# Kernel optimization log

Hardware: AMD Instinct MI355X
Metric: run time of the kernel (lower is better)

Reference implementation:

```python
import jax, jax.numpy as jnp
import numpy as np

B, SIZE, OUT = 32, 2048, 2048
EPS = 1e-5

def setup_inputs() -> dict:
    key = jax.random.key(0)
    ks = jax.random.split(key, 6)
    s = SIZE ** -0.5
    return {
        "x":    jax.random.normal(ks[0], (B, SIZE), jnp.float32),
        "Wq":   jax.random.normal(ks[1], (SIZE, SIZE), jnp.float32) * s,
        "Wk":   jax.random.normal(ks[2], (SIZE, SIZE), jnp.float32) * s,
        "Wv":   jax.random.normal(ks[3], (SIZE, SIZE), jnp.float32) * s,
        "p2":   jnp.zeros((5,), jnp.float32),              # OptimActivation params (activation2)
        "Wfc2": jax.random.normal(ks[4], (OUT, SIZE), jnp.float32) * s,
        "bfc2": jnp.zeros((OUT,), jnp.float32),
        "g2":   jnp.ones((OUT,), jnp.float32),             # LayerNorm2 weight
        "b2":   jnp.zeros((OUT,), jnp.float32),            # LayerNorm2 bias
    }

def _optim_activation(x, p):
    ps = jax.nn.softmax(p)
    # swish + sine + linear branches (sigmoid/tanh branches are computed but not summed in the original)
    return jax.nn.sigmoid(x) * x * ps[0] + jnp.sin(x) * ps[1] + x * ps[2]

def _layernorm(x, g, b):
    mu = jnp.mean(x, axis=-1, keepdims=True)
    var = jnp.mean(jnp.square(x - mu), axis=-1, keepdims=True)
    return (x - mu) * jax.lax.rsqrt(var + EPS) * g + b

def reference(x, Wq, Wk, Wv, p2, Wfc2, bfc2, g2, b2):
    q = x @ Wq.T                                   # [B, S]
    k = x @ Wk.T
    v = x @ Wv.T
    bsz, s = x.shape
    att = q[:, :, None] * k[:, None, :]            # outer product  [B, S, S]
    att = jax.nn.softmax(att.reshape(bsz, s * s), axis=-1).reshape(bsz, s, s)
    valued = jnp.einsum('bij,bj->bi', att, v)      # [B, S]
    # NOTE: original's activation/fc_linear/norm result is overwritten (dead code)
    fc = _optim_activation(valued, p2)
    fc = fc @ Wfc2.T + bfc2                        # [B, OUT]
    return _layernorm(fc, g2, b2)
```

## Files before the change

kernel.cpp:

```cpp
#include <hip/hip_runtime.h>
#include <hip/hip_bf16.h>


#define S 2048
#define BATCH 32

typedef __attribute__((ext_vector_type(8))) short short8;
typedef __attribute__((ext_vector_type(4))) float f32x4;

__device__ __forceinline__ void cvt8t(const float* __restrict__ p, short8& hi, short8& lo) {
  const float4* p4 = (const float4*)p;
  float4 a = p4[0], b = p4[1];
  float v[8] = {a.x, a.y, a.z, a.w, b.x, b.y, b.z, b.w};
#pragma unroll
  for (int t = 0; t < 8; ++t) {
    union { float f; unsigned u; } x; x.f = v[t];
    unsigned hb = x.u & 0xFFFF0000u;
    hi[t] = (short)(x.u >> 16);
    union { unsigned u; float f; } h; h.u = hb;
    union { float f; unsigned u; } l; l.f = v[t] - h.f;
    lo[t] = (short)(l.u >> 16);
  }
}

__global__ __launch_bounds__(512) void k_qkv(
    const float* __restrict__ x,
    const float* __restrict__ Wq,
    const float* __restrict__ Wk,
    const float* __restrict__ Wv,
    float* __restrict__ qkv) {
  int mi   = blockIdx.x >> 7;
  int nblk = blockIdx.x & 127;
  const float* W = (mi == 0) ? Wq : (mi == 1) ? Wk : Wv;
  float* out = qkv + mi * (BATCH * S);

  int tid  = threadIdx.x;
  int wave = tid >> 6;
  int lane = tid & 63;
  int lr   = lane & 15;
  int quad = lane >> 4;

  f32x4 acc0 = {0.f, 0.f, 0.f, 0.f};
  f32x4 acc1 = {0.f, 0.f, 0.f, 0.f};
  const float* wrow = W + (size_t)(nblk * 16 + lr) * S;
  const float* xr0  = x + (size_t)lr * S;
  const float* xr1  = x + (size_t)(lr + 16) * S;
  int kbase = wave * 256 + quad * 8;

#pragma unroll 2
  for (int ks = 0; ks < 8; ++ks) {
    int k0 = kbase + ks * 32;
    short8 bhi, blo, a0h, a0l, a1h, a1l;
    cvt8t(wrow + k0, bhi, blo);
    cvt8t(xr0 + k0, a0h, a0l);
    cvt8t(xr1 + k0, a1h, a1l);
    acc0 = __builtin_amdgcn_mfma_f32_16x16x32_bf16(a0h, bhi, acc0, 0, 0, 0);
    acc0 = __builtin_amdgcn_mfma_f32_16x16x32_bf16(a0l, bhi, acc0, 0, 0, 0);
    acc0 = __builtin_amdgcn_mfma_f32_16x16x32_bf16(a0h, blo, acc0, 0, 0, 0);
    acc1 = __builtin_amdgcn_mfma_f32_16x16x32_bf16(a1h, bhi, acc1, 0, 0, 0);
    acc1 = __builtin_amdgcn_mfma_f32_16x16x32_bf16(a1l, bhi, acc1, 0, 0, 0);
    acc1 = __builtin_amdgcn_mfma_f32_16x16x32_bf16(a1h, blo, acc1, 0, 0, 0);
  }

  __shared__ float red[8][64][8];
#pragma unroll
  for (int r = 0; r < 4; ++r) {
    red[wave][lane][r]     = acc0[r];
    red[wave][lane][4 + r] = acc1[r];
  }
  __syncthreads();
  if (tid < 64) {
    int lq = tid >> 4, lc = tid & 15;
    int n = nblk * 16 + lc;
#pragma unroll
    for (int r = 0; r < 8; ++r) {
      float s = 0.f;
#pragma unroll
      for (int w = 0; w < 8; ++w) s += red[w][tid][r];
      int m = (r < 4) ? (lq * 4 + r) : (16 + lq * 4 + (r - 4));
      out[m * S + n] = s;
    }
  }
}

__global__ __launch_bounds__(256) void k_attn(
    const float* __restrict__ qkv, float* __restrict__ Tout, float* __restrict__ Z) {
  int b    = blockIdx.x >> 5;
  int iblk = blockIdx.x & 31;
  const float* q = qkv + b * S;
  const float* k = qkv + BATCH * S + b * S;
  const float* v = qkv + 2 * BATCH * S + b * S;

  __shared__ __align__(16) float2 kv[S];
  __shared__ float redmx[4][4];
  __shared__ float redST[256][2];
  __shared__ float Msh;

  int tid = threadIdx.x;
  float qmx = -1e30f, qmn = 1e30f, kmx = -1e30f, kmn = 1e30f;
  for (int idx = tid; idx < S; idx += 256) {
    float kk = k[idx], vv = v[idx], qq = q[idx];
    kv[idx] = make_float2(kk, vv);
    qmx = fmaxf(qmx, qq); qmn = fminf(qmn, qq);
    kmx = fmaxf(kmx, kk); kmn = fminf(kmn, kk);
  }
  for (int off = 32; off; off >>= 1) {
    qmx = fmaxf(qmx, __shfl_xor(qmx, off));
    qmn = fminf(qmn, __shfl_xor(qmn, off));
    kmx = fmaxf(kmx, __shfl_xor(kmx, off));
    kmn = fminf(kmn, __shfl_xor(kmn, off));
  }
  int wave = tid >> 6, lane = tid & 63;
  if (lane == 0) {
    redmx[wave][0] = qmx; redmx[wave][1] = qmn;
    redmx[wave][2] = kmx; redmx[wave][3] = kmn;
  }
  __syncthreads();
  if (tid == 0) {
    float a = redmx[0][0], bn = redmx[0][1], c = redmx[0][2], d = redmx[0][3];
    for (int w = 1; w < 4; ++w) {
      a = fmaxf(a, redmx[w][0]); bn = fminf(bn, redmx[w][1]);
      c = fmaxf(c, redmx[w][2]); d = fminf(d, redmx[w][3]);
    }
    Msh = fmaxf(fmaxf(a * c, a * d), fmaxf(bn * c, bn * d));
  }
  __syncthreads();
  float M = Msh;

  const float LOG2E = 1.4426950408889634f;
  int i = iblk * 64 + lane;
  float aa = q[i] * LOG2E;
  float cc = -M * LOG2E;
  float Sacc = 0.f, Tacc = 0.f;
  int j0 = wave * 512;
#pragma unroll 8
  for (int j = j0; j < j0 + 512; j += 2) {
    float4 p = *(const float4*)&kv[j];
    float e0 = __builtin_amdgcn_exp2f(fmaf(aa, p.x, cc));
    float e1 = __builtin_amdgcn_exp2f(fmaf(aa, p.z, cc));
    Sacc += e0 + e1;
    Tacc = fmaf(e0, p.y, fmaf(e1, p.w, Tacc));
  }
  redST[tid][0] = Sacc;
  redST[tid][1] = Tacc;
  __syncthreads();
  if (tid < 64) {
    float Sf = redST[tid][0] + redST[tid + 64][0] + redST[tid + 128][0] + redST[tid + 192][0];
    float Tf = redST[tid][1] + redST[tid + 64][1] + redST[tid + 128][1] + redST[tid + 192][1];
    Tout[b * S + iblk * 64 + tid] = Tf;
    for (int off = 32; off; off >>= 1) Sf += __shfl_xor(Sf, off);
    if (tid == 0) atomicAdd(&Z[b], Sf);
  }
}

__global__ __launch_bounds__(256) void k_act(
    const float* __restrict__ Tin, const float* __restrict__ Z,
    const float* __restrict__ p2, float* __restrict__ fc) {
  int gid = blockIdx.x * 256 + threadIdx.x;
  int b = gid >> 11;
  const float LOG2E = 1.4426950408889634f;
  float p[5];
  float mx = -1e30f;
#pragma unroll
  for (int t = 0; t < 5; ++t) { p[t] = p2[t]; mx = fmaxf(mx, p[t]); }
  float se = 0.f;
#pragma unroll
  for (int t = 0; t < 5; ++t) { p[t] = __builtin_amdgcn_exp2f((p[t] - mx) * LOG2E); se += p[t]; }
  float inv = 1.f / se;
  float val = Tin[gid] / Z[b];
  float sig = __builtin_amdgcn_rcpf(1.f + __builtin_amdgcn_exp2f(-val * LOG2E));
  float sn  = __builtin_amdgcn_sinf(val * 0.15915494309189535f);
  fc[gid] = sig * val * (p[0] * inv) + sn * (p[1] * inv) + val * (p[2] * inv);
}

__global__ __launch_bounds__(512) void k_fc(
    const float* __restrict__ fc,
    const float* __restrict__ W,
    const float* __restrict__ bias,
    float* __restrict__ y) {
  int nblk = blockIdx.x;
  int tid  = threadIdx.x;
  int wave = tid >> 6;
  int lane = tid & 63;
  int lr   = lane & 15;
  int quad = lane >> 4;

  f32x4 acc0 = {0.f, 0.f, 0.f, 0.f};
  f32x4 acc1 = {0.f, 0.f, 0.f, 0.f};
  const float* wrow = W + (size_t)(nblk * 16 + lr) * S;
  const float* xr0  = fc + (size_t)lr * S;
  const float* xr1  = fc + (size_t)(lr + 16) * S;
  int kbase = wave * 256 + quad * 8;

#pragma unroll 2
  for (int ks = 0; ks < 8; ++ks) {
    int k0 = kbase + ks * 32;
    short8 bhi, blo, a0h, a0l, a1h, a1l;
    cvt8t(wrow + k0, bhi, blo);
    cvt8t(xr0 + k0, a0h, a0l);
    cvt8t(xr1 + k0, a1h, a1l);
    acc0 = __builtin_amdgcn_mfma_f32_16x16x32_bf16(a0h, bhi, acc0, 0, 0, 0);
    acc0 = __builtin_amdgcn_mfma_f32_16x16x32_bf16(a0l, bhi, acc0, 0, 0, 0);
    acc0 = __builtin_amdgcn_mfma_f32_16x16x32_bf16(a0h, blo, acc0, 0, 0, 0);
    acc1 = __builtin_amdgcn_mfma_f32_16x16x32_bf16(a1h, bhi, acc1, 0, 0, 0);
    acc1 = __builtin_amdgcn_mfma_f32_16x16x32_bf16(a1l, bhi, acc1, 0, 0, 0);
    acc1 = __builtin_amdgcn_mfma_f32_16x16x32_bf16(a1h, blo, acc1, 0, 0, 0);
  }

  __shared__ float red[8][64][8];
#pragma unroll
  for (int r = 0; r < 4; ++r) {
    red[wave][lane][r]     = acc0[r];
    red[wave][lane][4 + r] = acc1[r];
  }
  __syncthreads();
  if (tid < 64) {
    int lq = tid >> 4, lc = tid & 15;
    int n = nblk * 16 + lc;
    float bsum = bias[n];
#pragma unroll
    for (int r = 0; r < 8; ++r) {
      float s = 0.f;
#pragma unroll
      for (int w = 0; w < 8; ++w) s += red[w][tid][r];
      int m = (r < 4) ? (lq * 4 + r) : (16 + lq * 4 + (r - 4));
      y[m * S + n] = s + bsum;
    }
  }
}

__global__ __launch_bounds__(256) void k_ln(
    const float* __restrict__ y, const float* __restrict__ g,
    const float* __restrict__ bb, float* __restrict__ out) {
  int b = blockIdx.x;
  const float* row = y + b * S;
  float s = 0.f, s2 = 0.f;
  for (int i = threadIdx.x; i < S; i += 256) {
    float t = row[i];
    s += t; s2 += t * t;
  }
  for (int off = 32; off; off >>= 1) {
    s  += __shfl_xor(s, off);
    s2 += __shfl_xor(s2, off);
  }
  __shared__ float rs[4], rs2[4];
  __shared__ float mu_s, r_s;
  int wave = threadIdx.x >> 6, lane = threadIdx.x & 63;
  if (lane == 0) { rs[wave] = s; rs2[wave] = s2; }
  __syncthreads();
  if (threadIdx.x == 0) {
    float S1 = rs[0] + rs[1] + rs[2] + rs[3];
    float S2 = rs2[0] + rs2[1] + rs2[2] + rs2[3];
    float mu = S1 / (float)S;
    float var = S2 / (float)S - mu * mu;
    mu_s = mu;
    r_s = rsqrtf(var + 1e-5f);
  }
  __syncthreads();
  float mu = mu_s, r = r_s;
  for (int i = threadIdx.x; i < S; i += 256) {
    out[b * S + i] = (row[i] - mu) * r * g[i] + bb[i];
  }
}

extern "C" void kernel_launch(void* const* d_in, const int* in_sizes, int n_in,
                              void* d_out, int out_size, void* d_ws, size_t ws_size,
                              hipStream_t stream) {
  (void)in_sizes; (void)n_in; (void)out_size; (void)ws_size;
  const float* x    = (const float*)d_in[0];
  const float* Wq   = (const float*)d_in[1];
  const float* Wk   = (const float*)d_in[2];
  const float* Wv   = (const float*)d_in[3];
  const float* p2   = (const float*)d_in[4];
  const float* Wfc2 = (const float*)d_in[5];
  const float* bfc2 = (const float*)d_in[6];
  const float* g2   = (const float*)d_in[7];
  const float* b2   = (const float*)d_in[8];
  float* out = (float*)d_out;

  float* qkv = (float*)d_ws;
  float* T   = qkv + 3 * BATCH * S;
  float* Z   = T + BATCH * S;
  float* fc  = Z + 32;
  float* y   = fc + BATCH * S;

  hipMemsetAsync(Z, 0, 32 * sizeof(float), stream);
  k_qkv<<<384, 512, 0, stream>>>(x, Wq, Wk, Wv, qkv);
  k_attn<<<1024, 256, 0, stream>>>(qkv, T, Z);
  k_act<<<256, 256, 0, stream>>>(T, Z, p2, fc);
  k_fc<<<128, 512, 0, stream>>>(fc, Wfc2, bfc2, y);
  k_ln<<<32, 256, 0, stream>>>(y, g2, b2, out);
}
```

Measured before the change: 171.1 us.

## Split-K the QKV and FC GEMMs and drop atomics and memset for softmax sum

```diff
diff --git a/kernel.cpp b/kernel.cpp
--- a/kernel.cpp
+++ b/kernel.cpp
@@ -15,24 +15,25 @@
 #pragma unroll
   for (int t = 0; t < 8; ++t) {
     union { float f; unsigned u; } x; x.f = v[t];
-    unsigned hb = x.u & 0xFFFF0000u;
     hi[t] = (short)(x.u >> 16);
-    union { unsigned u; float f; } h; h.u = hb;
+    union { unsigned u; float f; } h; h.u = x.u & 0xFFFF0000u;
     union { float f; unsigned u; } l; l.f = v[t] - h.f;
     lo[t] = (short)(l.u >> 16);
   }
 }
 
-__global__ __launch_bounds__(512) void k_qkv(
+__global__ __launch_bounds__(256) void k_qkv(
     const float* __restrict__ x,
     const float* __restrict__ Wq,
     const float* __restrict__ Wk,
     const float* __restrict__ Wv,
-    float* __restrict__ qkv) {
-  int mi   = blockIdx.x >> 7;
-  int nblk = blockIdx.x & 127;
+    float* __restrict__ qkvp) {
+  int bid  = blockIdx.x;
+  int mi   = bid >> 8;
+  int kh   = (bid >> 7) & 1;
+  int nblk = bid & 127;
   const float* W = (mi == 0) ? Wq : (mi == 1) ? Wk : Wv;
-  float* out = qkv + mi * (BATCH * S);
+  float* out = qkvp + (size_t)kh * (3 * BATCH * S) + (size_t)mi * (BATCH * S);
 
   int tid  = threadIdx.x;
   int wave = tid >> 6;
@@ -45,7 +46,7 @@
   const float* wrow = W + (size_t)(nblk * 16 + lr) * S;
   const float* xr0  = x + (size_t)lr * S;
   const float* xr1  = x + (size_t)(lr + 16) * S;
-  int kbase = wave * 256 + quad * 8;
+  int kbase = kh * 1024 + wave * 256 + quad * 8;
 
 #pragma unroll 2
   for (int ks = 0; ks < 8; ++ks) {
@@ -62,7 +63,7 @@
     acc1 = __builtin_amdgcn_mfma_f32_16x16x32_bf16(a1h, blo, acc1, 0, 0, 0);
   }
 
-  __shared__ float red[8][64][8];
+  __shared__ float red[4][64][8];
 #pragma unroll
   for (int r = 0; r < 4; ++r) {
     red[wave][lane][r]     = acc0[r];
@@ -74,9 +75,7 @@
     int n = nblk * 16 + lc;
 #pragma unroll
     for (int r = 0; r < 8; ++r) {
-      float s = 0.f;
-#pragma unroll
-      for (int w = 0; w < 8; ++w) s += red[w][tid][r];
+      float s = red[0][tid][r] + red[1][tid][r] + red[2][tid][r] + red[3][tid][r];
       int m = (r < 4) ? (lq * 4 + r) : (16 + lq * 4 + (r - 4));
       out[m * S + n] = s;
     }
@@ -84,14 +83,18 @@
 }
 
 __global__ __launch_bounds__(256) void k_attn(
-    const float* __restrict__ qkv, float* __restrict__ Tout, float* __restrict__ Z) {
+    const float* __restrict__ qkvp, float* __restrict__ Tout, float* __restrict__ Spart) {
   int b    = blockIdx.x >> 5;
   int iblk = blockIdx.x & 31;
-  const float* q = qkv + b * S;
-  const float* k = qkv + BATCH * S + b * S;
-  const float* v = qkv + 2 * BATCH * S + b * S;
+  const float* qA = qkvp + (size_t)b * S;
+  const float* kA = qA + BATCH * S;
+  const float* vA = qA + 2 * BATCH * S;
+  const float* qB = qA + 3 * BATCH * S;
+  const float* kB = kA + 3 * BATCH * S;
+  const float* vB = vA + 3 * BATCH * S;
 
   __shared__ __align__(16) float2 kv[S];
+  __shared__ float qsh[64];
   __shared__ float redmx[4][4];
   __shared__ float redST[256][2];
   __shared__ float Msh;
@@ -99,8 +102,11 @@
   int tid = threadIdx.x;
   float qmx = -1e30f, qmn = 1e30f, kmx = -1e30f, kmn = 1e30f;
   for (int idx = tid; idx < S; idx += 256) {
-    float kk = k[idx], vv = v[idx], qq = q[idx];
+    float kk = kA[idx] + kB[idx];
+    float vv = vA[idx] + vB[idx];
+    float qq = qA[idx] + qB[idx];
     kv[idx] = make_float2(kk, vv);
+    if ((idx >> 6) == iblk) qsh[idx & 63] = qq;
     qmx = fmaxf(qmx, qq); qmn = fminf(qmn, qq);
     kmx = fmaxf(kmx, kk); kmn = fminf(kmn, kk);
   }
@@ -128,36 +134,50 @@
   float M = Msh;
 
   const float LOG2E = 1.4426950408889634f;
-  int i = iblk * 64 + lane;
-  float aa = q[i] * LOG2E;
+  float aa = qsh[lane] * LOG2E;
   float cc = -M * LOG2E;
-  float Sacc = 0.f, Tacc = 0.f;
+  float S0 = 0.f, S1 = 0.f, T0 = 0.f, T1 = 0.f;
   int j0 = wave * 512;
-#pragma unroll 8
-  for (int j = j0; j < j0 + 512; j += 2) {
-    float4 p = *(const float4*)&kv[j];
-    float e0 = __builtin_amdgcn_exp2f(fmaf(aa, p.x, cc));
-    float e1 = __builtin_amdgcn_exp2f(fmaf(aa, p.z, cc));
-    Sacc += e0 + e1;
-    Tacc = fmaf(e0, p.y, fmaf(e1, p.w, Tacc));
-  }
-  redST[tid][0] = Sacc;
-  redST[tid][1] = Tacc;
+#pragma unroll 4
+  for (int j = j0; j < j0 + 512; j += 4) {
+    float4 p0 = *(const float4*)&kv[j];
+    float4 p1 = *(const float4*)&kv[j + 2];
+    float e0 = __builtin_amdgcn_exp2f(fmaf(aa, p0.x, cc));
+    float e1 = __builtin_amdgcn_exp2f(fmaf(aa, p0.z, cc));
+    float e2 = __builtin_amdgcn_exp2f(fmaf(aa, p1.x, cc));
+    float e3 = __builtin_amdgcn_exp2f(fmaf(aa, p1.z, cc));
+    S0 += e0 + e1;
+    S1 += e2 + e3;
+    T0 = fmaf(e0, p0.y, fmaf(e1, p0.w, T0));
+    T1 = fmaf(e2, p1.y, fmaf(e3, p1.w, T1));
+  }
+  redST[tid][0] = S0 + S1;
+  redST[tid][1] = T0 + T1;
   __syncthreads();
   if (tid < 64) {
     float Sf = redST[tid][0] + redST[tid + 64][0] + redST[tid + 128][0] + redST[tid + 192][0];
     float Tf = redST[tid][1] + redST[tid + 64][1] + redST[tid + 128][1] + redST[tid + 192][1];
     Tout[b * S + iblk * 64 + tid] = Tf;
     for (int off = 32; off; off >>= 1) Sf += __shfl_xor(Sf, off);
-    if (tid == 0) atomicAdd(&Z[b], Sf);
+    if (tid == 0) Spart[b * 32 + iblk] = Sf;
   }
 }
 
 __global__ __launch_bounds__(256) void k_act(
-    const float* __restrict__ Tin, const float* __restrict__ Z,
+    const float* __restrict__ Tin, const float* __restrict__ Spart,
     const float* __restrict__ p2, float* __restrict__ fc) {
-  int gid = blockIdx.x * 256 + threadIdx.x;
+  int tid = threadIdx.x;
+  int gid = blockIdx.x * 256 + tid;
   int b = gid >> 11;
+  __shared__ float Zsh;
+  if (tid < 64) {
+    float zv = (tid < 32) ? Spart[b * 32 + tid] : 0.f;
+    for (int off = 32; off; off >>= 1) zv += __shfl_xor(zv, off);
+    if (tid == 0) Zsh = zv;
+  }
+  __syncthreads();
+  float Z = Zsh;
+
   const float LOG2E = 1.4426950408889634f;
   float p[5];
   float mx = -1e30f;
@@ -167,7 +187,7 @@
 #pragma unroll
   for (int t = 0; t < 5; ++t) { p[t] = __builtin_amdgcn_exp2f((p[t] - mx) * LOG2E); se += p[t]; }
   float inv = 1.f / se;
-  float val = Tin[gid] / Z[b];
+  float val = Tin[gid] / Z;
   float sig = __builtin_amdgcn_rcpf(1.f + __builtin_amdgcn_exp2f(-val * LOG2E));
   float sn  = __builtin_amdgcn_sinf(val * 0.15915494309189535f);
   fc[gid] = sig * val * (p[0] * inv) + sn * (p[1] * inv) + val * (p[2] * inv);
@@ -176,9 +196,10 @@
 __global__ __launch_bounds__(512) void k_fc(
     const float* __restrict__ fc,
     const float* __restrict__ W,
-    const float* __restrict__ bias,
-    float* __restrict__ y) {
-  int nblk = blockIdx.x;
+    float* __restrict__ yp) {
+  int bid  = blockIdx.x;
+  int kh   = bid >> 7;
+  int nblk = bid & 127;
   int tid  = threadIdx.x;
   int wave = tid >> 6;
   int lane = tid & 63;
@@ -190,10 +211,10 @@
   const float* wrow = W + (size_t)(nblk * 16 + lr) * S;
   const float* xr0  = fc + (size_t)lr * S;
   const float* xr1  = fc + (size_t)(lr + 16) * S;
-  int kbase = wave * 256 + quad * 8;
-
-#pragma unroll 2
-  for (int ks = 0; ks < 8; ++ks) {
+  int kbase = kh * 1024 + wave * 128 + quad * 8;
+
+#pragma unroll
+  for (int ks = 0; ks < 4; ++ks) {
     int k0 = kbase + ks * 32;
     short8 bhi, blo, a0h, a0l, a1h, a1l;
     cvt8t(wrow + k0, bhi, blo);
@@ -217,26 +238,31 @@
   if (tid < 64) {
     int lq = tid >> 4, lc = tid & 15;
     int n = nblk * 16 + lc;
-    float bsum = bias[n];
 #pragma unroll
     for (int r = 0; r < 8; ++r) {
       float s = 0.f;
 #pragma unroll
       for (int w = 0; w < 8; ++w) s += red[w][tid][r];
       int m = (r < 4) ? (lq * 4 + r) : (16 + lq * 4 + (r - 4));
-      y[m * S + n] = s + bsum;
+      yp[(size_t)kh * BATCH * S + m * S + n] = s;
     }
   }
 }
 
 __global__ __launch_bounds__(256) void k_ln(
-    const float* __restrict__ y, const float* __restrict__ g,
-    const float* __restrict__ bb, float* __restrict__ out) {
+    const float* __restrict__ yp, const float* __restrict__ bias,
+    const float* __restrict__ g, const float* __restrict__ bb,
+    float* __restrict__ out) {
   int b = blockIdx.x;
-  const float* row = y + b * S;
+  const float* r0 = yp + (size_t)b * S;
+  const float* r1 = r0 + BATCH * S;
+  float t8[8];
   float s = 0.f, s2 = 0.f;
-  for (int i = threadIdx.x; i < S; i += 256) {
-    float t = row[i];
+#pragma unroll
+  for (int it = 0; it < 8; ++it) {
+    int i = threadIdx.x + it * 256;
+    float t = r0[i] + r1[i] + bias[i];
+    t8[it] = t;
     s += t; s2 += t * t;
   }
   for (int off = 32; off; off >>= 1) {
@@ -258,8 +284,10 @@
   }
   __syncthreads();
   float mu = mu_s, r = r_s;
-  for (int i = threadIdx.x; i < S; i += 256) {
-    out[b * S + i] = (row[i] - mu) * r * g[i] + bb[i];
+#pragma unroll
+  for (int it = 0; it < 8; ++it) {
+    int i = threadIdx.x + it * 256;
+    out[b * S + i] = (t8[it] - mu) * r * g[i] + bb[i];
   }
 }
 
@@ -278,16 +306,15 @@
   const float* b2   = (const float*)d_in[8];
   float* out = (float*)d_out;
 
-  float* qkv = (float*)d_ws;
-  float* T   = qkv + 3 * BATCH * S;
-  float* Z   = T + BATCH * S;
-  float* fc  = Z + 32;
-  float* y   = fc + BATCH * S;
-
-  hipMemsetAsync(Z, 0, 32 * sizeof(float), stream);
-  k_qkv<<<384, 512, 0, stream>>>(x, Wq, Wk, Wv, qkv);
-  k_attn<<<1024, 256, 0, stream>>>(qkv, T, Z);
-  k_act<<<256, 256, 0, stream>>>(T, Z, p2, fc);
-  k_fc<<<128, 512, 0, stream>>>(fc, Wfc2, bfc2, y);
-  k_ln<<<32, 256, 0, stream>>>(y, g2, b2, out);
-}
+  float* qkvp  = (float*)d_ws;
+  float* T     = qkvp + 2 * 3 * BATCH * S;
+  float* Spart = T + BATCH * S;
+  float* fc    = Spart + BATCH * 32;
+  float* yp    = fc + BATCH * S;
+
+  k_qkv<<<768, 256, 0, stream>>>(x, Wq, Wk, Wv, qkvp);
+  k_attn<<<1024, 256, 0, stream>>>(qkvp, T, Spart);
+  k_act<<<256, 256, 0, stream>>>(T, Spart, p2, fc);
+  k_fc<<<256, 512, 0, stream>>>(fc, Wfc2, yp);
+  k_ln<<<32, 256, 0, stream>>>(yp, bfc2, g2, b2, out);
+}
```

New measurement: 152.7 us. 10.7% less time.
